# Kernel tuning notes

Measured on AMD Instinct MI355X. Metric: run time of the kernel, lower is better.

## Reference

```python
import jax, jax.numpy as jnp
import numpy as np

N, D_IN, D_OUT, E = 8192, 1024, 1024, 8

def setup_inputs() -> dict:
    key = jax.random.key(0)
    ks = jax.random.split(key, 5)
    x = jax.random.normal(ks[0], (N, D_IN), dtype=jnp.float32)
    # expert weights stacked: [E, D_IN, D_OUT], bias [E, D_OUT]
    We = jax.random.normal(ks[1], (E, D_IN, D_OUT), dtype=jnp.float32) / np.sqrt(D_IN)
    be = jax.random.normal(ks[2], (E, D_OUT), dtype=jnp.float32) * 0.01
    # gating net: Linear(D_IN -> E)
    Wg = jax.random.normal(ks[3], (D_IN, E), dtype=jnp.float32) / np.sqrt(D_IN)
    bg = jax.random.normal(ks[4], (E,), dtype=jnp.float32) * 0.01
    return {"x": x, "We": We, "be": be, "Wg": Wg, "bg": bg}

def reference(x, We, be, Wg, bg):
    # gate: softmax over experts  [N, E]
    gate_probs = jax.nn.softmax(x @ Wg + bg, axis=-1)
    # all experts run densely on every token: [N, E, D_OUT]
    expert_out = jnp.einsum('ni,eio->neo', x, We) + be[None, :, :]
    # gate-weighted sum over experts: [N, D_OUT]
    return jnp.einsum('neo,ne->no', expert_out, gate_probs)
```

## Files before the change

kernel.cpp:

```cpp
#include <hip/hip_runtime.h>
#include <hip/hip_bf16.h>

#define N_TOK 8192
#define DIN   1024
#define DOUT  1024
#define NE    8
#define KTOT  (NE * DIN)
#define BM    256
#define BN    128
#define NKH   (KTOT / 32)

typedef __attribute__((ext_vector_type(4))) float f32x4;
typedef __attribute__((ext_vector_type(8))) short short8;
typedef unsigned int u32;

__device__ __forceinline__ ushort f2bf(float f) {
    u32 u = __float_as_uint(f);
    u32 r = (u + 0x7fffu + ((u >> 16) & 1u)) >> 16;
    return (ushort)r;
}

__device__ __forceinline__ void gload_lds16(const void* gp, void* lp) {
    __builtin_amdgcn_global_load_lds(
        (const __attribute__((address_space(1))) u32*)gp,
        (__attribute__((address_space(3))) u32*)lp, 16, 0, 0);
}

#define PH_BAR()  __builtin_amdgcn_s_barrier()
#define LGKM0()   asm volatile("s_waitcnt lgkmcnt(0)" ::: "memory")
#define LGKM8()   asm volatile("s_waitcnt lgkmcnt(8)" ::: "memory")
#define VMCNT3()  asm volatile("s_waitcnt vmcnt(3)" ::: "memory")
#define VMCNT0()  asm volatile("s_waitcnt vmcnt(0)" ::: "memory")
#define SBAR0()   __builtin_amdgcn_sched_barrier(0)

__global__ void gate_kernel(const float* __restrict__ x, const float* __restrict__ Wg,
                            const float* __restrict__ bg, float* __restrict__ g) {
    int w = threadIdx.x >> 6, lane = threadIdx.x & 63;
    int n = blockIdx.x * 4 + w;
    const float* xr = x + (size_t)n * DIN;
    float p[NE];
#pragma unroll
    for (int e = 0; e < NE; ++e) p[e] = 0.f;
    for (int i = lane; i < DIN; i += 64) {
        float xv = xr[i];
        const float* wr_ = Wg + i * NE;
#pragma unroll
        for (int e = 0; e < NE; ++e) p[e] = fmaf(xv, wr_[e], p[e]);
    }
#pragma unroll
    for (int off = 32; off > 0; off >>= 1) {
#pragma unroll
        for (int e = 0; e < NE; ++e) p[e] += __shfl_down(p[e], off);
    }
    if (lane == 0) {
        float l2[NE], m = -1e30f;
#pragma unroll
        for (int e = 0; e < NE; ++e) { l2[e] = p[e] + bg[e]; m = fmaxf(m, l2[e]); }
        float s = 0.f;
#pragma unroll
        for (int e = 0; e < NE; ++e) { l2[e] = expf(l2[e] - m); s += l2[e]; }
        float inv = 1.f / s;
#pragma unroll
        for (int e = 0; e < NE; ++e) g[n * NE + e] = l2[e] * inv;
    }
}

__global__ void cvt_x_kernel(const float* __restrict__ x, ushort* __restrict__ xb) {
    int idx = blockIdx.x * 256 + threadIdx.x;
    float4 v = ((const float4*)x)[idx];
    ushort4 o = make_ushort4(f2bf(v.x), f2bf(v.y), f2bf(v.z), f2bf(v.w));
    ((ushort4*)xb)[idx] = o;
}

__global__ void transpose_w_kernel(const float* __restrict__ We, ushort* __restrict__ BT) {
    __shared__ float tile[64][65];
    int kb = blockIdx.x * 64, ob = blockIdx.y * 64;
    int t = threadIdx.x;
#pragma unroll
    for (int ph = 0; ph < 16; ++ph) {
        int idx = ph * 256 + t;
        int r = idx >> 6, c = idx & 63;
        tile[r][c] = We[(size_t)(kb + r) * DOUT + ob + c];
    }
    __syncthreads();
#pragma unroll
    for (int ph = 0; ph < 16; ++ph) {
        int idx = ph * 256 + t;
        int r = idx >> 6, c = idx & 63;
        BT[(size_t)(ob + r) * KTOT + kb + c] = f2bf(tile[c][r]);
    }
}

__global__ __launch_bounds__(512, 2) void moe_gemm(
    const ushort* __restrict__ xb,
    const ushort* __restrict__ BT,
    const float*  __restrict__ g,
    const float*  __restrict__ be,
    float*        __restrict__ out)
{
    __shared__ __align__(16) ushort Al[4][BM * 32];
    __shared__ __align__(16) ushort Bl[4][BN * 32];
    __shared__ __align__(16) float  gLds[BM][NE];

    int bid = blockIdx.x;
    int swz = (bid & 7) * 32 + (bid >> 3);
    int colb = swz & 7;
    int rowb = swz >> 3;
    int brow = rowb * BM, bcol = colb * BN;

    int tid = threadIdx.x;
    int w = tid >> 6, lane = tid & 63;
    int wm = w >> 1, wn = w & 1;
    int ro = lane & 15, gq = lane >> 4;
    int jrow = gq * 4;

    float4 gv = ((const float4*)(g + (size_t)brow * NE))[tid];
    ((float4*)&gLds[0][0])[tid] = gv;

    int offA[4], offB[4];
#pragma unroll
    for (int m = 0; m < 4; ++m) {
        int r = wm * 64 + m * 16 + ro;
        offA[m] = r * 32 + ((gq * 8) ^ ((r & 6) << 2));
    }
#pragma unroll
    for (int n = 0; n < 4; ++n) {
        int c = wn * 64 + n * 16 + ro;
        offB[n] = c * 32 + ((gq * 8) ^ ((c & 6) << 2));
    }

    auto stA = [&](int s, int K) {
#pragma unroll
        for (int L = 0; L < 2; ++L) {
            int chunk = L * 512 + tid;
            int row = chunk >> 2, slot = chunk & 3;
            int ks = (slot * 8) ^ ((row & 6) << 2);
            int ka = (K * 32) & (DIN - 1);
            gload_lds16(xb + (size_t)(brow + row) * DIN + ka + ks,
                        (char*)&Al[s][0] + (size_t)(chunk & ~63) * 16);
        }
    };
    auto stB = [&](int s, int K) {
        int chunk = tid;
        int row = chunk >> 2, slot = chunk & 3;
        int ks = (slot * 8) ^ ((row & 6) << 2);
        gload_lds16(BT + (size_t)(bcol + row) * KTOT + K * 32 + ks,
                    (char*)&Bl[s][0] + (size_t)(chunk & ~63) * 16);
    };

    f32x4 accP[4][4];
    u32   accB[4][4][2];
    short8 fA[2][4], fB[2][4];
#pragma unroll
    for (int m = 0; m < 4; ++m)
#pragma unroll
        for (int n = 0; n < 4; ++n) {
            accP[m][n] = (f32x4){0.f, 0.f, 0.f, 0.f};
            accB[m][n][0] = 0u; accB[m][n][1] = 0u;
        }

    auto fold = [&](int e) {
#pragma unroll
        for (int m = 0; m < 4; ++m) {
            int rbase = wm * 64 + m * 16 + jrow;
            float g0 = gLds[rbase + 0][e], g1 = gLds[rbase + 1][e];
            float g2 = gLds[rbase + 2][e], g3 = gLds[rbase + 3][e];
#pragma unroll
            for (int n = 0; n < 4; ++n) {
                u32 p0 = accB[m][n][0];
                float lo0 = __uint_as_float(p0 << 16)         + g0 * accP[m][n][0];
                float hi0 = __uint_as_float(p0 & 0xffff0000u) + g1 * accP[m][n][1];
                accB[m][n][0] = (u32)f2bf(lo0) | ((u32)f2bf(hi0) << 16);
                u32 p1 = accB[m][n][1];
                float lo1 = __uint_as_float(p1 << 16)         + g2 * accP[m][n][2];
                float hi1 = __uint_as_float(p1 & 0xffff0000u) + g3 * accP[m][n][3];
                accB[m][n][1] = (u32)f2bf(lo1) | ((u32)f2bf(hi1) << 16);
                accP[m][n] = (f32x4){0.f, 0.f, 0.f, 0.f};
            }
        }
    };

#define LD_FRAGS(SET, RBUF) do {                                              \
    const ushort* _As = &Al[RBUF][0];                                         \
    const ushort* _Bs = &Bl[RBUF][0];                                         \
    _Pragma("unroll") for (int _m = 0; _m < 4; ++_m)                          \
        fA[SET][_m] = *(const short8*)(_As + offA[_m]);                       \
    _Pragma("unroll") for (int _n = 0; _n < 4; ++_n)                          \
        fB[SET][_n] = *(const short8*)(_Bs + offB[_n]);                       \
} while (0)

#define DO_MFMA(SET) do {                                                     \
    __builtin_amdgcn_s_setprio(1);                                            \
    _Pragma("unroll") for (int _m = 0; _m < 4; ++_m) {                        \
        accP[_m][0] = __builtin_amdgcn_mfma_f32_16x16x32_bf16(fA[SET][_m], fB[SET][0], accP[_m][0], 0, 0, 0); \
        accP[_m][1] = __builtin_amdgcn_mfma_f32_16x16x32_bf16(fA[SET][_m], fB[SET][1], accP[_m][1], 0, 0, 0); \
        accP[_m][2] = __builtin_amdgcn_mfma_f32_16x16x32_bf16(fA[SET][_m], fB[SET][2], accP[_m][2], 0, 0, 0); \
        accP[_m][3] = __builtin_amdgcn_mfma_f32_16x16x32_bf16(fA[SET][_m], fB[SET][3], accP[_m][3], 0, 0, 0); \
    }                                                                         \
    __builtin_amdgcn_s_setprio(0);                                            \
} while (0)

    stA(0, 0); stB(0, 0);
    stA(1, 1); stB(1, 1);
    stA(2, 2); stB(2, 2);
    VMCNT3();
    PH_BAR();
    LD_FRAGS(0, 0);

    for (int it = 0; it < 63; ++it) {
        int k = it * 4;
        LD_FRAGS(1, 1); stA(3, k + 3); stB(3, k + 3);
        LGKM8(); SBAR0(); DO_MFMA(0); VMCNT3(); PH_BAR();
        LD_FRAGS(0, 2); stA(0, k + 4); stB(0, k + 4);
        LGKM8(); SBAR0(); DO_MFMA(1); VMCNT3(); PH_BAR();
        LD_FRAGS(1, 3); stA(1, k + 5); stB(1, k + 5);
        LGKM8(); SBAR0(); DO_MFMA(0); VMCNT3(); PH_BAR();
        LD_FRAGS(0, 0); stA(2, k + 6); stB(2, k + 6);
        LGKM8(); SBAR0(); DO_MFMA(1);
        if ((it & 7) == 7) fold(it >> 3);
        VMCNT3(); PH_BAR();
    }

    LD_FRAGS(1, 1); stA(3, 255); stB(3, 255);
    LGKM8(); SBAR0(); DO_MFMA(0); VMCNT3(); PH_BAR();
    LD_FRAGS(0, 2);
    LGKM8(); SBAR0(); DO_MFMA(1); VMCNT0(); PH_BAR();
    LD_FRAGS(1, 3);
    LGKM8(); SBAR0(); DO_MFMA(0); PH_BAR();
    LGKM0(); SBAR0(); DO_MFMA(1);

#undef LD_FRAGS
#undef DO_MFMA

#pragma unroll
    for (int m = 0; m < 4; ++m) {
#pragma unroll
        for (int j = 0; j < 4; ++j) {
            int lrow = wm * 64 + m * 16 + jrow + j;
            int grow = brow + lrow;
            float g8[NE];
#pragma unroll
            for (int e = 0; e < NE; ++e) g8[e] = gLds[lrow][e];
#pragma unroll
            for (int n = 0; n < 4; ++n) {
                int col = bcol + wn * 64 + n * 16 + ro;
                float bias = 0.f;
#pragma unroll
                for (int e = 0; e < NE; ++e) bias = fmaf(g8[e], be[e * DOUT + col], bias);
                u32 p = accB[m][n][j >> 1];
                float base = __uint_as_float((j & 1) ? (p & 0xffff0000u) : (p << 16));
                out[(size_t)grow * DOUT + col] = base + g8[7] * accP[m][n][j] + bias;
            }
        }
    }
}

extern "C" void kernel_launch(void* const* d_in, const int* in_sizes, int n_in,
                              void* d_out, int out_size, void* d_ws, size_t ws_size,
                              hipStream_t stream) {
    const float* x  = (const float*)d_in[0];
    const float* We = (const float*)d_in[1];
    const float* be = (const float*)d_in[2];
    const float* Wg = (const float*)d_in[3];
    const float* bg = (const float*)d_in[4];
    float* out = (float*)d_out;

    char* ws = (char*)d_ws;
    float*  gbuf = (float*)ws;
    ushort* xb   = (ushort*)(ws + (size_t)256 * 1024);
    ushort* BT   = (ushort*)(ws + (size_t)256 * 1024 + (size_t)N_TOK * DIN * 2);

    gate_kernel<<<N_TOK / 4, 256, 0, stream>>>(x, Wg, bg, gbuf);
    cvt_x_kernel<<<(N_TOK * DIN / 4) / 256, 256, 0, stream>>>(x, xb);
    transpose_w_kernel<<<dim3(KTOT / 64, DOUT / 64), 256, 0, stream>>>(We, BT);
    moe_gemm<<<(N_TOK / BM) * (DOUT / BN), 512, 0, stream>>>(xb, BT, gbuf, be, out);
}
```

Baseline: 197.0 us.

## Load B fragments directly from global into registers, bypassing LDS

Drops the LDS staging buffer for the expert-weight (B) operand. Each wave now issues direct global loads of its B fragments into a double-buffered register set two k-steps ahead, and the vmcnt and lgkmcnt waits are retuned to match. This removes B's LDS writes, reads and footprint, which may allow better occupancy. In exchange, the two waves that share a column tile both fetch the same B data from global or L2 with no sharing, and the direct loads are less coalesced (16 bytes per lane on rows strided by KTOT).

```diff
diff --git a/kernel.cpp b/kernel.cpp
--- a/kernel.cpp
+++ b/kernel.cpp
@@ -28,8 +28,9 @@
 
 #define PH_BAR()  __builtin_amdgcn_s_barrier()
 #define LGKM0()   asm volatile("s_waitcnt lgkmcnt(0)" ::: "memory")
-#define LGKM8()   asm volatile("s_waitcnt lgkmcnt(8)" ::: "memory")
-#define VMCNT3()  asm volatile("s_waitcnt vmcnt(3)" ::: "memory")
+#define LGKM4()   asm volatile("s_waitcnt lgkmcnt(4)" ::: "memory")
+#define VMCNT6()  asm volatile("s_waitcnt vmcnt(6)" ::: "memory")
+#define VMCNT4()  asm volatile("s_waitcnt vmcnt(4)" ::: "memory")
 #define VMCNT0()  asm volatile("s_waitcnt vmcnt(0)" ::: "memory")
 #define SBAR0()   __builtin_amdgcn_sched_barrier(0)
 
@@ -99,7 +100,6 @@
     float*        __restrict__ out)
 {
     __shared__ __align__(16) ushort Al[4][BM * 32];
-    __shared__ __align__(16) ushort Bl[4][BN * 32];
     __shared__ __align__(16) float  gLds[BM][NE];
 
     int bid = blockIdx.x;
@@ -117,16 +117,17 @@
     float4 gv = ((const float4*)(g + (size_t)brow * NE))[tid];
     ((float4*)&gLds[0][0])[tid] = gv;
 
-    int offA[4], offB[4];
+    int offA[4];
 #pragma unroll
     for (int m = 0; m < 4; ++m) {
         int r = wm * 64 + m * 16 + ro;
         offA[m] = r * 32 + ((gq * 8) ^ ((r & 6) << 2));
     }
+    const ushort* bBase[4];
 #pragma unroll
     for (int n = 0; n < 4; ++n) {
-        int c = wn * 64 + n * 16 + ro;
-        offB[n] = c * 32 + ((gq * 8) ^ ((c & 6) << 2));
+        int c = bcol + wn * 64 + n * 16 + ro;
+        bBase[n] = BT + (size_t)c * KTOT + gq * 8;
     }
 
     auto stA = [&](int s, int K) {
@@ -140,17 +141,10 @@
                         (char*)&Al[s][0] + (size_t)(chunk & ~63) * 16);
         }
     };
-    auto stB = [&](int s, int K) {
-        int chunk = tid;
-        int row = chunk >> 2, slot = chunk & 3;
-        int ks = (slot * 8) ^ ((row & 6) << 2);
-        gload_lds16(BT + (size_t)(bcol + row) * KTOT + K * 32 + ks,
-                    (char*)&Bl[s][0] + (size_t)(chunk & ~63) * 16);
-    };
 
     f32x4 accP[4][4];
     u32   accB[4][4][2];
-    short8 fA[2][4], fB[2][4];
+    short8 fA[2][4], bReg[2][4];
 #pragma unroll
     for (int m = 0; m < 4; ++m)
 #pragma unroll
@@ -182,54 +176,68 @@
 
 #define LD_FRAGS(SET, RBUF) do {                                              \
     const ushort* _As = &Al[RBUF][0];                                         \
-    const ushort* _Bs = &Bl[RBUF][0];                                         \
     _Pragma("unroll") for (int _m = 0; _m < 4; ++_m)                          \
         fA[SET][_m] = *(const short8*)(_As + offA[_m]);                       \
+} while (0)
+
+#define ISSUE_B(SET, KP) do {                                                 \
     _Pragma("unroll") for (int _n = 0; _n < 4; ++_n)                          \
-        fB[SET][_n] = *(const short8*)(_Bs + offB[_n]);                       \
+        bReg[SET][_n] = *(const short8*)(bBase[_n] + (size_t)(KP) * 32);      \
 } while (0)
 
 #define DO_MFMA(SET) do {                                                     \
     __builtin_amdgcn_s_setprio(1);                                            \
     _Pragma("unroll") for (int _m = 0; _m < 4; ++_m) {                        \
-        accP[_m][0] = __builtin_amdgcn_mfma_f32_16x16x32_bf16(fA[SET][_m], fB[SET][0], accP[_m][0], 0, 0, 0); \
-        accP[_m][1] = __builtin_amdgcn_mfma_f32_16x16x32_bf16(fA[SET][_m], fB[SET][1], accP[_m][1], 0, 0, 0); \
-        accP[_m][2] = __builtin_amdgcn_mfma_f32_16x16x32_bf16(fA[SET][_m], fB[SET][2], accP[_m][2], 0, 0, 0); \
-        accP[_m][3] = __builtin_amdgcn_mfma_f32_16x16x32_bf16(fA[SET][_m], fB[SET][3], accP[_m][3], 0, 0, 0); \
+        accP[_m][0] = __builtin_amdgcn_mfma_f32_16x16x32_bf16(fA[SET][_m], bReg[SET][0], accP[_m][0], 0, 0, 0); \
+        accP[_m][1] = __builtin_amdgcn_mfma_f32_16x16x32_bf16(fA[SET][_m], bReg[SET][1], accP[_m][1], 0, 0, 0); \
+        accP[_m][2] = __builtin_amdgcn_mfma_f32_16x16x32_bf16(fA[SET][_m], bReg[SET][2], accP[_m][2], 0, 0, 0); \
+        accP[_m][3] = __builtin_amdgcn_mfma_f32_16x16x32_bf16(fA[SET][_m], bReg[SET][3], accP[_m][3], 0, 0, 0); \
     }                                                                         \
     __builtin_amdgcn_s_setprio(0);                                            \
 } while (0)
 
-    stA(0, 0); stB(0, 0);
-    stA(1, 1); stB(1, 1);
-    stA(2, 2); stB(2, 2);
-    VMCNT3();
+    stA(0, 0); stA(1, 1); stA(2, 2);
+    ISSUE_B(0, 0); ISSUE_B(1, 1);
+    VMCNT4();
     PH_BAR();
     LD_FRAGS(0, 0);
 
     for (int it = 0; it < 63; ++it) {
         int k = it * 4;
-        LD_FRAGS(1, 1); stA(3, k + 3); stB(3, k + 3);
-        LGKM8(); SBAR0(); DO_MFMA(0); VMCNT3(); PH_BAR();
-        LD_FRAGS(0, 2); stA(0, k + 4); stB(0, k + 4);
-        LGKM8(); SBAR0(); DO_MFMA(1); VMCNT3(); PH_BAR();
-        LD_FRAGS(1, 3); stA(1, k + 5); stB(1, k + 5);
-        LGKM8(); SBAR0(); DO_MFMA(0); VMCNT3(); PH_BAR();
-        LD_FRAGS(0, 0); stA(2, k + 6); stB(2, k + 6);
-        LGKM8(); SBAR0(); DO_MFMA(1);
+        LD_FRAGS(1, 1); stA(3, k + 3);
+        LGKM4(); SBAR0(); DO_MFMA(0);
+        ISSUE_B(0, k + 2);
+        VMCNT6(); PH_BAR();
+        LD_FRAGS(0, 2); stA(0, k + 4);
+        LGKM4(); SBAR0(); DO_MFMA(1);
+        ISSUE_B(1, k + 3);
+        VMCNT6(); PH_BAR();
+        LD_FRAGS(1, 3); stA(1, k + 5);
+        LGKM4(); SBAR0(); DO_MFMA(0);
+        ISSUE_B(0, k + 4);
+        VMCNT6(); PH_BAR();
+        LD_FRAGS(0, 0); stA(2, k + 6);
+        LGKM4(); SBAR0(); DO_MFMA(1);
+        ISSUE_B(1, k + 5);
         if ((it & 7) == 7) fold(it >> 3);
-        VMCNT3(); PH_BAR();
-    }
-
-    LD_FRAGS(1, 1); stA(3, 255); stB(3, 255);
-    LGKM8(); SBAR0(); DO_MFMA(0); VMCNT3(); PH_BAR();
+        VMCNT6(); PH_BAR();
+    }
+
+    LD_FRAGS(1, 1); stA(3, 255);
+    LGKM4(); SBAR0(); DO_MFMA(0);
+    ISSUE_B(0, 254);
+    VMCNT6(); PH_BAR();
     LD_FRAGS(0, 2);
-    LGKM8(); SBAR0(); DO_MFMA(1); VMCNT0(); PH_BAR();
+    LGKM4(); SBAR0(); DO_MFMA(1);
+    ISSUE_B(1, 255);
+    VMCNT4(); PH_BAR();
     LD_FRAGS(1, 3);
-    LGKM8(); SBAR0(); DO_MFMA(0); PH_BAR();
+    LGKM4(); SBAR0(); DO_MFMA(0);
+    VMCNT0(); PH_BAR();
     LGKM0(); SBAR0(); DO_MFMA(1);
 
 #undef LD_FRAGS
+#undef ISSUE_B
 #undef DO_MFMA
 
 #pragma unroll
```

After: 350.6 us. +78.0%, slower.
